# Performance work log

Hardware: AMD Instinct MI355X
Metric: run time of the kernel (lower is better)

Reference implementation:

```python
import jax, jax.numpy as jnp
import numpy as np

B, L, D, T, V, H = 32, 48, 768, 32, 30522, 768

def build_iou_mask_map():
    # Faithful to the __init__ construction: banded validity mask [32, 33].
    m = np.zeros((32, 33), dtype=np.float32)
    for i in range(0, 32, 1):
        m[i, i + 1:min(i + 17, 33)] = 1.0
    for i in range(0, 32 - 16, 2):
        m[i, list(range(18 + i, 33, 2))] = 1.0
    return jnp.asarray(m)

def setup_inputs() -> dict:
    key = jax.random.key(0)
    ks = jax.random.split(key, 6)
    s = 0.02  # xavier-ish init scale
    return {
        'hidden_states_text': jax.random.normal(ks[0], (B, L, D), jnp.float32),
        'hidden_states_object': jax.random.normal(ks[1], (B, T + 1, D), jnp.float32),
        'w_t1': jax.random.normal(ks[2], (D, H), jnp.float32) * s,
        'b_t1': jnp.zeros((H,), jnp.float32),
        'w_t2': jax.random.normal(ks[3], (H, V), jnp.float32) * s,
        'b_t2': jnp.zeros((V,), jnp.float32),
        'w_i1': jax.random.normal(ks[4], (3 * D, H), jnp.float32) * s,
        'b_i1': jnp.zeros((H,), jnp.float32),
        'w_i2': jax.random.normal(ks[5], (H, 3), jnp.float32) * s,
        'b_i2': jnp.zeros((3,), jnp.float32),
    }

def reference(hidden_states_text, hidden_states_object,
              w_t1, b_t1, w_t2, b_t2, w_i1, b_i1, w_i2, b_i2):
    # final_mlp: Dropout(eval: id) -> Linear -> ReLU -> Dropout -> Linear
    logits_text = jax.nn.relu(hidden_states_text @ w_t1 + b_t1) @ w_t2 + b_t2  # [B,L,V]

    hc = hidden_states_object                # [B, T+1, D]
    t = hc.shape[1] - 1
    s_idx = jnp.arange(t)                    # [T]
    e_idx = jnp.arange(t + 1)                # [T+1]
    # (0.5*(s+e)).long() == floor division for non-negative ints
    c_idx = (s_idx[:, None] + e_idx[None, :]) // 2          # [T, T+1]
    c_point = hc[:, c_idx, :]                                # [B, T, T+1, D] gather
    d = hc.shape[-1]
    s_pts = jnp.broadcast_to(hc[:, :-1, None, :], (hc.shape[0], t, t + 1, d))
    e_pts = jnp.broadcast_to(hc[:, None, :, :], (hc.shape[0], t, t + 1, d))
    sce = jnp.concatenate([s_pts, c_point, e_pts], axis=-1)  # [B, T, T+1, 3D]

    # final_mlp_3: Linear(3D->H) -> ReLU -> Dropout(id) -> Linear(H->3)
    h = jax.nn.relu(jnp.einsum('bstf,fh->bsth', sce, w_i1) + b_i1)
    logits_iou = jnp.einsum('bsth,hk->bstk', h, w_i2) + b_i2  # [B,T,T+1,3]
    logits_iou = jnp.transpose(logits_iou, (0, 3, 1, 2))      # [B,3,T,T+1]

    return logits_text, logits_iou, build_iou_mask_map()
```

## Files before the change

### kernel.cpp

```cpp
#include <hip/hip_runtime.h>

typedef unsigned short u16;
typedef short v8s __attribute__((ext_vector_type(8)));
typedef float v4f __attribute__((ext_vector_type(4)));

#define KDIM 768
#define M_TEXT 1536
#define N_VOCAB 30522
#define N_VOCAB_PAD 30592
#define M_HC 1056
#define M_HC_PAD 1152
#define N_IOU 2304
#define OUT_IOU_OFF 46881792
#define OUT_MASK_OFF 46983168

__device__ __forceinline__ u16 f2bf(float f) {
  unsigned u = __float_as_uint(f);
  u += 0x7fffu + ((u >> 16) & 1u);
  return (u16)(u >> 16);
}

__global__ __launch_bounds__(256) void prep_cvt(const float* __restrict__ xt_in,
                                                const float* __restrict__ hc_in,
                                                u16* __restrict__ xt,
                                                u16* __restrict__ hcb,
                                                float* __restrict__ out) {
  const int NXT = M_TEXT * KDIM / 4;
  if (blockIdx.x >= 2016) {
    int idx = (blockIdx.x - 2016) * 256 + threadIdx.x;
    if (idx >= 1056) return;
    int i = idx / 33, j = idx % 33;
    float v = 0.f;
    int hi = min(i + 17, 33);
    if (j >= i + 1 && j < hi) v = 1.f;
    if ((i & 1) == 0 && i < 16 && j >= 18 + i && ((j - (18 + i)) & 1) == 0) v = 1.f;
    out[OUT_MASK_OFF + idx] = v;
    return;
  }
  int i = blockIdx.x * 256 + threadIdx.x;
  if (i < NXT) {
    float4 v = ((const float4*)xt_in)[i];
    ushort4 o; o.x = f2bf(v.x); o.y = f2bf(v.y); o.z = f2bf(v.z); o.w = f2bf(v.w);
    ((ushort4*)xt)[i] = o;
  } else {
    int j = i - NXT;
    int row = j / 192;
    float4 v = make_float4(0.f, 0.f, 0.f, 0.f);
    if (row < M_HC) v = ((const float4*)hc_in)[j];
    ushort4 o; o.x = f2bf(v.x); o.y = f2bf(v.y); o.z = f2bf(v.z); o.w = f2bf(v.w);
    ((ushort4*)hcb)[j] = o;
  }
}

__global__ __launch_bounds__(256) void transpose_all(const float* __restrict__ w_t1,
                                                     u16* __restrict__ w_t1T,
                                                     const float* __restrict__ w_t2,
                                                     u16* __restrict__ w_t2T,
                                                     const float* __restrict__ w_i1,
                                                     u16* __restrict__ w_i1T) {
  __shared__ float tile[64][65];
  int b = blockIdx.x;
  const float* ip; u16* op; int C, bx, by;
  if (b < 144) {
    ip = w_t1; op = w_t1T; C = 768; bx = b % 12; by = b / 12;
  } else if (b < 5880) {
    int r = b - 144; ip = w_t2; op = w_t2T; C = N_VOCAB; bx = r % 12; by = r / 12;
  } else {
    int r = b - 5880; int z = r / 144; int q = r % 144;
    ip = w_i1 + (long)z * 768 * 768; op = w_i1T + (long)z * 768 * 768;
    C = 768; bx = q % 12; by = q / 12;
  }
  int r0 = bx * 64, c0 = by * 64;
  int tx = threadIdx.x & 63, tg = threadIdx.x >> 6;
#pragma unroll
  for (int i = 0; i < 16; ++i) {
    int r = tg + i * 4;
    int gc = c0 + tx;
    tile[r][tx] = (gc < C) ? ip[(long)(r0 + r) * C + gc] : 0.f;
  }
  __syncthreads();
#pragma unroll
  for (int i = 0; i < 16; ++i) {
    int cc = tg + i * 4;
    op[(long)(c0 + cc) * KDIM + r0 + tx] = f2bf(tile[tx][cc]);
  }
}

__global__ __launch_bounds__(256)
void gemm_small(const u16* __restrict__ xt, const u16* __restrict__ w_t1T,
                u16* __restrict__ htext, const float* __restrict__ b_t1,
                const u16* __restrict__ hcb, const u16* __restrict__ w_i1T,
                float* __restrict__ Xcat) {
  __shared__ u16 sA[128 * 32];
  __shared__ u16 sB[128 * 32];
  const int b = blockIdx.x;
  const u16 *A, *BT;
  float* fout = nullptr;
  u16* bfout = nullptr;
  const float* bias = nullptr;
  int mode, bx, by, ldc;
  if (b < 72) {
    mode = 1; bx = b % 6; by = b / 6;
    A = xt; BT = w_t1T; bfout = htext; bias = b_t1; ldc = KDIM;
  } else {
    int r = b - 72;
    mode = 2; bx = r % 18; by = r / 18;
    A = hcb; BT = w_i1T; fout = Xcat; ldc = N_IOU;
  }
  const int tid = threadIdx.x;
  const int wid = tid >> 6;
  const int lane = tid & 63;
  const int lrow = lane & 15;
  const int quad = lane >> 4;
  const int wm = (wid & 1) * 64;
  const int wn = (wid >> 1) * 64;
  const int m0 = by * 128;
  const int n0 = bx * 128;

  const int srow = wid * 32 + (lane >> 2);
  const int scol = (lane & 3) * 8;
  const u16* gA = A + (long)(m0 + srow) * KDIM + scol;
  const u16* gB = BT + (long)(n0 + srow) * KDIM + scol;
  u16* lA = &sA[(wid * 32) * 32];
  u16* lB = &sB[(wid * 32) * 32];

  v4f acc[4][4];
#pragma unroll
  for (int i = 0; i < 4; ++i)
#pragma unroll
    for (int j = 0; j < 4; ++j) acc[i][j] = (v4f){0.f, 0.f, 0.f, 0.f};

  const v8s* pA = (const v8s*)sA;
  const v8s* pB = (const v8s*)sB;
  const int ia0 = (wm + lrow) * 4 + quad;
  const int ib0 = (wn + lrow) * 4 + quad;

  for (int kt = 0; kt < KDIM / 32; ++kt) {
    const u16* ga = gA + kt * 32;
    const u16* gb = gB + kt * 32;
    __builtin_amdgcn_global_load_lds((const __attribute__((address_space(1))) void*)ga,
                                     (__attribute__((address_space(3))) void*)lA, 16, 0, 0);
    __builtin_amdgcn_global_load_lds((const __attribute__((address_space(1))) void*)(ga + 16 * KDIM),
                                     (__attribute__((address_space(3))) void*)(lA + 16 * 32), 16, 0, 0);
    __builtin_amdgcn_global_load_lds((const __attribute__((address_space(1))) void*)gb,
                                     (__attribute__((address_space(3))) void*)lB, 16, 0, 0);
    __builtin_amdgcn_global_load_lds((const __attribute__((address_space(1))) void*)(gb + 16 * KDIM),
                                     (__attribute__((address_space(3))) void*)(lB + 16 * 32), 16, 0, 0);
    __syncthreads();

    v8s af[4], bfr[4];
#pragma unroll
    for (int mt = 0; mt < 4; ++mt) af[mt] = pA[ia0 + mt * 64];
#pragma unroll
    for (int nt = 0; nt < 4; ++nt) bfr[nt] = pB[ib0 + nt * 64];
#pragma unroll
    for (int mt = 0; mt < 4; ++mt)
#pragma unroll
      for (int nt = 0; nt < 4; ++nt)
        acc[mt][nt] = __builtin_amdgcn_mfma_f32_16x16x32_bf16(af[mt], bfr[nt], acc[mt][nt], 0, 0, 0);
    __syncthreads();
  }

#pragma unroll
  for (int nt = 0; nt < 4; ++nt) {
    int c = n0 + wn + nt * 16 + lrow;
    float bv = 0.f;
    if (mode == 1) bv = bias[c];
#pragma unroll
    for (int mt = 0; mt < 4; ++mt) {
#pragma unroll
      for (int r = 0; r < 4; ++r) {
        int row = m0 + wm + mt * 16 + quad * 4 + r;
        float v = acc[mt][nt][r] + bv;
        if (mode == 1) {
          bfout[(long)row * ldc + c] = f2bf(fmaxf(v, 0.f));
        } else {
          fout[(long)row * ldc + c] = v;
        }
      }
    }
  }
}

#define DSREAD_B(sB) do {                                                  \
    const u16* _b = (sB) + bBase;                                          \
    _Pragma("unroll")                                                      \
    for (int _nf = 0; _nf < 4; ++_nf) {                                    \
      bfr[_nf][0] = *(const v8s*)(_b + _nf * 1024 + c0);                   \
      bfr[_nf][1] = *(const v8s*)(_b + _nf * 1024 + c1);                   \
    } } while (0)

#define DSREAD_A(sA, q) do {                                               \
    const u16* _a = (sA) + aBase + (q) * 2048;                             \
    af[0][0] = *(const v8s*)(_a + c0);                                     \
    af[0][1] = *(const v8s*)(_a + c1);                                     \
    af[1][0] = *(const v8s*)(_a + 1024 + c0);                              \
    af[1][1] = *(const v8s*)(_a + 1024 + c1);                              \
  } while (0)

#define MFMA_Q(q) do {                                                     \
    _Pragma("unroll")                                                      \
    for (int _m = 0; _m < 2; ++_m)                                         \
      _Pragma("unroll")                                                    \
      for (int _nf = 0; _nf < 4; ++_nf) {                                  \
        acc[2*(q)+_m][_nf] = __builtin_amdgcn_mfma_f32_16x16x32_bf16(      \
            af[_m][0], bfr[_nf][0], acc[2*(q)+_m][_nf], 0, 0, 0);          \
        acc[2*(q)+_m][_nf] = __builtin_amdgcn_mfma_f32_16x16x32_bf16(      \
            af[_m][1], bfr[_nf][1], acc[2*(q)+_m][_nf], 0, 0, 0);          \
      } } while (0)

#define BAR_SB() do { __builtin_amdgcn_s_barrier();                        \
                      __builtin_amdgcn_sched_barrier(0); } while (0)
#define LGKM0() do { asm volatile("s_waitcnt lgkmcnt(0)" ::: "memory");    \
                     __builtin_amdgcn_sched_barrier(0); } while (0)

__global__ __launch_bounds__(512, 2)
void gemm_big(const u16* __restrict__ A, const u16* __restrict__ BT,
              float* __restrict__ out, const float* __restrict__ bias) {
  __shared__ u16 sbuf[2][2][256 * 64];

  const int id = blockIdx.x;
  const int swz = (id & 7) * 90 + (id >> 3);
  const int mt = swz % 6;
  const int nt = swz / 6;
  const int m0 = mt * 256, n0 = nt * 256;

  const int tid = threadIdx.x;
  const int wid = tid >> 6;
  const int lane = tid & 63;
  const int l3 = lane >> 3;
  const int l7 = lane & 7;
  const int lrow = lane & 15;
  const int quad = lane >> 4;
  const int wr = wid >> 2;
  const int wc = wid & 3;

  const int xc = (l7 ^ l3) * 8;
  const u16* Ag = A  + (long)(m0 + wid * 16 + l3) * KDIM + xc;
  const u16* Bg = BT + (long)(n0 + wid * 16 + l3) * KDIM + xc;

  u16* const sA0 = &sbuf[0][0][0];
  u16* const sB0 = &sbuf[0][1][0];
  u16* const sA1 = &sbuf[1][0][0];
  u16* const sB1 = &sbuf[1][1][0];

  auto stageA = [&](u16* sdst, int kt, int h) {
#pragma unroll
    for (int j = 0; j < 2; ++j)
      __builtin_amdgcn_global_load_lds(
          (const __attribute__((address_space(1))) void*)(Ag + (long)kt * 64 +
                                                          (long)((h * 128 + j * 8) * KDIM)),
          (__attribute__((address_space(3))) void*)(sdst + (h * 128 + wid * 16 + j * 8) * 64),
          16, 0, 0);
  };
  auto stageB = [&](u16* sdst, int kt, int h) {
    const int hh = (n0 + h * 128 >= N_VOCAB_PAD) ? 0 : h;
#pragma unroll
    for (int j = 0; j < 2; ++j)
      __builtin_amdgcn_global_load_lds(
          (const __attribute__((address_space(1))) void*)(Bg + (long)kt * 64 +
                                                          (long)((hh * 128 + j * 8) * KDIM)),
          (__attribute__((address_space(3))) void*)(sdst + (h * 128 + wid * 16 + j * 8) * 64),
          16, 0, 0);
  };

  const int aBase = (wr * 128 + lrow) * 64;
  const int bBase = (wc * 64 + lrow) * 64;
  const int xls = (lrow & 7) * 8;
  const int c0 = (quad * 8) ^ xls;
  const int c1 = c0 ^ 32;

  v4f acc[8][4];
#pragma unroll
  for (int i = 0; i < 8; ++i)
#pragma unroll
    for (int j = 0; j < 4; ++j) acc[i][j] = (v4f){0.f, 0.f, 0.f, 0.f};

  v8s bfr[4][2];
  v8s af[2][2];

  stageA(sA0, 0, 0); stageA(sA0, 0, 1);
  stageB(sB0, 0, 0); stageB(sB0, 0, 1);
  stageB(sB1, 1, 0); stageB(sB1, 1, 1);
  asm volatile("s_waitcnt vmcnt(4)" ::: "memory");
  __builtin_amdgcn_sched_barrier(0);
  BAR_SB();

#pragma unroll 1
  for (int it = 0; it < 6; ++it) {
    const int kA1 = 2 * it + 1;
    const int kB0 = 2 * it + 2;
    const int kB1 = 2 * it + 3;
    const bool more = (it < 5);

    DSREAD_B(sB0);
    DSREAD_A(sA0, 0);
    stageA(sA1, kA1, 0);
    __builtin_amdgcn_s_barrier();
    LGKM0();
    __builtin_amdgcn_s_setprio(1); MFMA_Q(0); __builtin_amdgcn_s_setprio(0);
    BAR_SB();

    DSREAD_A(sA0, 1);
    stageA(sA1, kA1, 1);
    __builtin_amdgcn_s_barrier();
    LGKM0();
    __builtin_amdgcn_s_setprio(1); MFMA_Q(1); __builtin_amdgcn_s_setprio(0);
    BAR_SB();

    DSREAD_A(sA0, 2);
    if (more) stageB(sB0, kB0, 0);
    __builtin_amdgcn_s_barrier();
    LGKM0();
    __builtin_amdgcn_s_setprio(1); MFMA_Q(2); __builtin_amdgcn_s_setprio(0);
    BAR_SB();

    DSREAD_A(sA0, 3);
    if (more) stageB(sB0, kB0, 1);
    __builtin_amdgcn_s_barrier();
    LGKM0();
    __builtin_amdgcn_s_setprio(1); MFMA_Q(3); __builtin_amdgcn_s_setprio(0);
    if (more) { asm volatile("s_waitcnt vmcnt(4)" ::: "memory"); }
    else      { asm volatile("s_waitcnt vmcnt(0)" ::: "memory"); }
    __builtin_amdgcn_sched_barrier(0);
    BAR_SB();

    DSREAD_B(sB1);
    DSREAD_A(sA1, 0);
    if (more) stageA(sA0, kB0, 0);
    __builtin_amdgcn_s_barrier();
    LGKM0();
    __builtin_amdgcn_s_setprio(1); MFMA_Q(0); __builtin_amdgcn_s_setprio(0);
    BAR_SB();

    DSREAD_A(sA1, 1);
    if (more) stageA(sA0, kB0, 1);
    __builtin_amdgcn_s_barrier();
    LGKM0();
    __builtin_amdgcn_s_setprio(1); MFMA_Q(1); __builtin_amdgcn_s_setprio(0);
    BAR_SB();

    DSREAD_A(sA1, 2);
    if (more) stageB(sB1, kB1, 0);
    __builtin_amdgcn_s_barrier();
    LGKM0();
    __builtin_amdgcn_s_setprio(1); MFMA_Q(2); __builtin_amdgcn_s_setprio(0);
    BAR_SB();

    DSREAD_A(sA1, 3);
    if (more) stageB(sB1, kB1, 1);
    __builtin_amdgcn_s_barrier();
    LGKM0();
    __builtin_amdgcn_s_setprio(1); MFMA_Q(3); __builtin_amdgcn_s_setprio(0);
    if (more) { asm volatile("s_waitcnt vmcnt(4)" ::: "memory");
                __builtin_amdgcn_sched_barrier(0); }
    BAR_SB();
  }

#pragma unroll
  for (int nf = 0; nf < 4; ++nf) {
    const int c = n0 + wc * 64 + nf * 16 + lrow;
    if (c < N_VOCAB) {
      const float bv = bias[c];
#pragma unroll
      for (int mf = 0; mf < 8; ++mf) {
        const long r0 = m0 + wr * 128 + mf * 16 + quad * 4;
#pragma unroll
        for (int rr = 0; rr < 4; ++rr)
          out[(r0 + rr) * (long)N_VOCAB + c] = acc[mf][nf][rr] + bv;
      }
    }
  }
}

#undef DSREAD_B
#undef DSREAD_A
#undef MFMA_Q
#undef BAR_SB
#undef LGKM0

__global__ __launch_bounds__(256) void iou_combine(const float* __restrict__ Xcat,
                                                   const float* __restrict__ b1,
                                                   const float* __restrict__ w2,
                                                   const float* __restrict__ b2,
                                                   float* __restrict__ out) {
  int gw = (blockIdx.x * 256 + threadIdx.x) >> 6;
  int lane = threadIdx.x & 63;
  if (gw >= 32 * 32 * 33) return;
  int b = gw / 1056;
  int rem = gw % 1056;
  int s = rem / 33;
  int t = rem % 33;
  int cidx = (s + t) >> 1;
  const float* ps = Xcat + (long)(b * 33 + s) * N_IOU;
  const float* pc = Xcat + (long)(b * 33 + cidx) * N_IOU + 768;
  const float* pe = Xcat + (long)(b * 33 + t) * N_IOU + 1536;
  float a0 = 0.f, a1 = 0.f, a2 = 0.f;
#pragma unroll
  for (int j = 0; j < 3; ++j) {
    int h0 = j * 256 + lane * 4;
    float4 vs = *(const float4*)(ps + h0);
    float4 vc = *(const float4*)(pc + h0);
    float4 ve = *(const float4*)(pe + h0);
    float4 vb = *(const float4*)(b1 + h0);
    const float* fs = (const float*)&vs;
    const float* fc = (const float*)&vc;
    const float* fe = (const float*)&ve;
    const float* fb = (const float*)&vb;
#pragma unroll
    for (int c = 0; c < 4; ++c) {
      float v = fmaxf(fs[c] + fc[c] + fe[c] + fb[c], 0.f);
      int h = h0 + c;
      a0 += v * w2[h * 3 + 0];
      a1 += v * w2[h * 3 + 1];
      a2 += v * w2[h * 3 + 2];
    }
  }
#pragma unroll
  for (int off = 32; off > 0; off >>= 1) {
    a0 += __shfl_down(a0, off, 64);
    a1 += __shfl_down(a1, off, 64);
    a2 += __shfl_down(a2, off, 64);
  }
  if (lane == 0) {
    int base = OUT_IOU_OFF + b * 3168 + s * 33 + t;
    out[base + 0 * 1056] = a0 + b2[0];
    out[base + 1 * 1056] = a1 + b2[1];
    out[base + 2 * 1056] = a2 + b2[2];
  }
}

extern "C" void kernel_launch(void* const* d_in, const int* in_sizes, int n_in,
                              void* d_out, int out_size, void* d_ws, size_t ws_size,
                              hipStream_t stream) {
  const float* hst  = (const float*)d_in[0];
  const float* hso  = (const float*)d_in[1];
  const float* w_t1 = (const float*)d_in[2];
  const float* b_t1 = (const float*)d_in[3];
  const float* w_t2 = (const float*)d_in[4];
  const float* b_t2 = (const float*)d_in[5];
  const float* w_i1 = (const float*)d_in[6];
  const float* b_i1 = (const float*)d_in[7];
  const float* w_i2 = (const float*)d_in[8];
  const float* b_i2 = (const float*)d_in[9];
  float* out = (float*)d_out;

  char* ws = (char*)d_ws;
  u16*   w_t2T = (u16*)(ws + 0);
  u16*   xt    = (u16*)(ws + 46989312);
  u16*   w_t1T = (u16*)(ws + 49348608);
  u16*   htext = (u16*)(ws + 50528256);
  u16*   hcb   = (u16*)(ws + 52887552);
  u16*   w_i1T = (u16*)(ws + 54657024);
  float* Xcat  = (float*)(ws + 58195968);

  prep_cvt<<<dim3(2021), dim3(256), 0, stream>>>(hst, hso, xt, hcb, out);
  transpose_all<<<dim3(6312), dim3(256), 0, stream>>>(w_t1, w_t1T, w_t2, w_t2T, w_i1, w_i1T);

  gemm_small<<<dim3(234), dim3(256), 0, stream>>>(xt, w_t1T, htext, b_t1, hcb, w_i1T, Xcat);

  gemm_big<<<dim3(720), dim3(512), 0, stream>>>(htext, w_t2T, out, b_t2);
  iou_combine<<<dim3(8448), dim3(256), 0, stream>>>(Xcat, b_i1, w_i2, b_i2, out);
}
```

Baseline: 506.9 us.

## Merge five launches into three with independent work co-scheduled per kernel

The stages are regrouped by dependency into three launches instead of five. The small weight transposes join the input conversion kernel. The large vocab-weight transpose is placed in the same grid as the small GEMMs. The IoU combine runs as extra blocks of the big text GEMM. This cuts launch gaps and lets independent work fill idle CUs during tail phases, at the cost of mixing block types that compete for resources and of larger shared-memory and register footprints in the merged kernels.

```diff
diff --git a/kernel.cpp b/kernel.cpp
--- a/kernel.cpp
+++ b/kernel.cpp
@@ -20,14 +20,56 @@
   return (u16)(u >> 16);
 }
 
-__global__ __launch_bounds__(256) void prep_cvt(const float* __restrict__ xt_in,
-                                                const float* __restrict__ hc_in,
-                                                u16* __restrict__ xt,
-                                                u16* __restrict__ hcb,
-                                                float* __restrict__ out) {
+__device__ __forceinline__ void transpose_body(const float* __restrict__ ip,
+                                               u16* __restrict__ op,
+                                               int C, int bx, int by,
+                                               float (*tile)[65]) {
+  int r0 = bx * 64, c0 = by * 64;
+  int tx = threadIdx.x & 63, tg = threadIdx.x >> 6;
+#pragma unroll
+  for (int i = 0; i < 16; ++i) {
+    int r = tg + i * 4;
+    int gc = c0 + tx;
+    tile[r][tx] = (gc < C) ? ip[(long)(r0 + r) * C + gc] : 0.f;
+  }
+  __syncthreads();
+#pragma unroll
+  for (int i = 0; i < 16; ++i) {
+    int cc = tg + i * 4;
+    op[(long)(c0 + cc) * KDIM + r0 + tx] = f2bf(tile[tx][cc]);
+  }
+}
+
+__global__ __launch_bounds__(256) void prep_and_smallT(const float* __restrict__ xt_in,
+                                                       const float* __restrict__ hc_in,
+                                                       u16* __restrict__ xt,
+                                                       u16* __restrict__ hcb,
+                                                       float* __restrict__ out,
+                                                       const float* __restrict__ w_t1,
+                                                       u16* __restrict__ w_t1T,
+                                                       const float* __restrict__ w_i1,
+                                                       u16* __restrict__ w_i1T) {
+  __shared__ float tile[64][65];
   const int NXT = M_TEXT * KDIM / 4;
-  if (blockIdx.x >= 2016) {
-    int idx = (blockIdx.x - 2016) * 256 + threadIdx.x;
+  const int b = blockIdx.x;
+  if (b < 2016) {
+    int i = b * 256 + threadIdx.x;
+    if (i < NXT) {
+      float4 v = ((const float4*)xt_in)[i];
+      ushort4 o; o.x = f2bf(v.x); o.y = f2bf(v.y); o.z = f2bf(v.z); o.w = f2bf(v.w);
+      ((ushort4*)xt)[i] = o;
+    } else {
+      int j = i - NXT;
+      int row = j / 192;
+      float4 v = make_float4(0.f, 0.f, 0.f, 0.f);
+      if (row < M_HC) v = ((const float4*)hc_in)[j];
+      ushort4 o; o.x = f2bf(v.x); o.y = f2bf(v.y); o.z = f2bf(v.z); o.w = f2bf(v.w);
+      ((ushort4*)hcb)[j] = o;
+    }
+    return;
+  }
+  if (b < 2021) {
+    int idx = (b - 2016) * 256 + threadIdx.x;
     if (idx >= 1056) return;
     int i = idx / 33, j = idx % 33;
     float v = 0.f;
@@ -37,73 +79,44 @@
     out[OUT_MASK_OFF + idx] = v;
     return;
   }
-  int i = blockIdx.x * 256 + threadIdx.x;
-  if (i < NXT) {
-    float4 v = ((const float4*)xt_in)[i];
-    ushort4 o; o.x = f2bf(v.x); o.y = f2bf(v.y); o.z = f2bf(v.z); o.w = f2bf(v.w);
-    ((ushort4*)xt)[i] = o;
-  } else {
-    int j = i - NXT;
-    int row = j / 192;
-    float4 v = make_float4(0.f, 0.f, 0.f, 0.f);
-    if (row < M_HC) v = ((const float4*)hc_in)[j];
-    ushort4 o; o.x = f2bf(v.x); o.y = f2bf(v.y); o.z = f2bf(v.z); o.w = f2bf(v.w);
-    ((ushort4*)hcb)[j] = o;
-  }
-}
-
-__global__ __launch_bounds__(256) void transpose_all(const float* __restrict__ w_t1,
-                                                     u16* __restrict__ w_t1T,
-                                                     const float* __restrict__ w_t2,
-                                                     u16* __restrict__ w_t2T,
-                                                     const float* __restrict__ w_i1,
-                                                     u16* __restrict__ w_i1T) {
-  __shared__ float tile[64][65];
-  int b = blockIdx.x;
-  const float* ip; u16* op; int C, bx, by;
-  if (b < 144) {
-    ip = w_t1; op = w_t1T; C = 768; bx = b % 12; by = b / 12;
-  } else if (b < 5880) {
-    int r = b - 144; ip = w_t2; op = w_t2T; C = N_VOCAB; bx = r % 12; by = r / 12;
-  } else {
-    int r = b - 5880; int z = r / 144; int q = r % 144;
-    ip = w_i1 + (long)z * 768 * 768; op = w_i1T + (long)z * 768 * 768;
-    C = 768; bx = q % 12; by = q / 12;
-  }
-  int r0 = bx * 64, c0 = by * 64;
-  int tx = threadIdx.x & 63, tg = threadIdx.x >> 6;
-#pragma unroll
-  for (int i = 0; i < 16; ++i) {
-    int r = tg + i * 4;
-    int gc = c0 + tx;
-    tile[r][tx] = (gc < C) ? ip[(long)(r0 + r) * C + gc] : 0.f;
-  }
-  __syncthreads();
-#pragma unroll
-  for (int i = 0; i < 16; ++i) {
-    int cc = tg + i * 4;
-    op[(long)(c0 + cc) * KDIM + r0 + tx] = f2bf(tile[tx][cc]);
+  if (b < 2165) {
+    int r = b - 2021;
+    transpose_body(w_t1, w_t1T, 768, r % 12, r / 12, tile);
+    return;
+  }
+  {
+    int r = b - 2165;
+    int z = r / 144, q = r % 144;
+    transpose_body(w_i1 + (long)z * 768 * 768, w_i1T + (long)z * 768 * 768,
+                   768, q % 12, q / 12, tile);
   }
 }
 
 __global__ __launch_bounds__(256)
-void gemm_small(const u16* __restrict__ xt, const u16* __restrict__ w_t1T,
-                u16* __restrict__ htext, const float* __restrict__ b_t1,
-                const u16* __restrict__ hcb, const u16* __restrict__ w_i1T,
-                float* __restrict__ Xcat) {
-  __shared__ u16 sA[128 * 32];
-  __shared__ u16 sB[128 * 32];
-  const int b = blockIdx.x;
+void midwork(const u16* __restrict__ xt, const u16* __restrict__ w_t1T,
+             u16* __restrict__ htext, const float* __restrict__ b_t1,
+             const u16* __restrict__ hcb, const u16* __restrict__ w_i1T,
+             float* __restrict__ Xcat,
+             const float* __restrict__ w_t2, u16* __restrict__ w_t2T) {
+  __shared__ char smem[64 * 65 * 4];
+  const int blk = blockIdx.x;
+  if (blk >= 234) {
+    int r = blk - 234;
+    transpose_body(w_t2, w_t2T, N_VOCAB, r % 12, r / 12, (float (*)[65])smem);
+    return;
+  }
+  u16* sA = (u16*)smem;
+  u16* sB = (u16*)(smem + 8192);
   const u16 *A, *BT;
   float* fout = nullptr;
   u16* bfout = nullptr;
   const float* bias = nullptr;
   int mode, bx, by, ldc;
-  if (b < 72) {
-    mode = 1; bx = b % 6; by = b / 6;
+  if (blk < 72) {
+    mode = 1; bx = blk % 6; by = blk / 6;
     A = xt; BT = w_t1T; bfout = htext; bias = b_t1; ldc = KDIM;
   } else {
-    int r = b - 72;
+    int r = blk - 72;
     mode = 2; bx = r % 18; by = r / 18;
     A = hcb; BT = w_i1T; fout = Xcat; ldc = N_IOU;
   }
@@ -215,9 +228,62 @@
                      __builtin_amdgcn_sched_barrier(0); } while (0)
 
 __global__ __launch_bounds__(512, 2)
-void gemm_big(const u16* __restrict__ A, const u16* __restrict__ BT,
-              float* __restrict__ out, const float* __restrict__ bias) {
+void bigwork(const u16* __restrict__ A, const u16* __restrict__ BT,
+             float* __restrict__ out, const float* __restrict__ bias,
+             const float* __restrict__ Xcat, const float* __restrict__ b1,
+             const float* __restrict__ w2, const float* __restrict__ b2) {
   __shared__ u16 sbuf[2][2][256 * 64];
+
+  const int tid = threadIdx.x;
+  const int wid = tid >> 6;
+  const int lane = tid & 63;
+
+  if (blockIdx.x >= 720) {
+    int gw = (blockIdx.x - 720) * 8 + wid;
+    if (gw >= 32 * 32 * 33) return;
+    int b = gw / 1056;
+    int rem = gw % 1056;
+    int s = rem / 33;
+    int t = rem % 33;
+    int cidx = (s + t) >> 1;
+    const float* ps = Xcat + (long)(b * 33 + s) * N_IOU;
+    const float* pc = Xcat + (long)(b * 33 + cidx) * N_IOU + 768;
+    const float* pe = Xcat + (long)(b * 33 + t) * N_IOU + 1536;
+    float a0 = 0.f, a1 = 0.f, a2 = 0.f;
+#pragma unroll
+    for (int j = 0; j < 3; ++j) {
+      int h0 = j * 256 + lane * 4;
+      float4 vs = *(const float4*)(ps + h0);
+      float4 vc = *(const float4*)(pc + h0);
+      float4 ve = *(const float4*)(pe + h0);
+      float4 vb = *(const float4*)(b1 + h0);
+      const float* fs = (const float*)&vs;
+      const float* fc = (const float*)&vc;
+      const float* fe = (const float*)&ve;
+      const float* fb = (const float*)&vb;
+#pragma unroll
+      for (int c = 0; c < 4; ++c) {
+        float v = fmaxf(fs[c] + fc[c] + fe[c] + fb[c], 0.f);
+        int h = h0 + c;
+        a0 += v * w2[h * 3 + 0];
+        a1 += v * w2[h * 3 + 1];
+        a2 += v * w2[h * 3 + 2];
+      }
+    }
+#pragma unroll
+    for (int off = 32; off > 0; off >>= 1) {
+      a0 += __shfl_down(a0, off, 64);
+      a1 += __shfl_down(a1, off, 64);
+      a2 += __shfl_down(a2, off, 64);
+    }
+    if (lane == 0) {
+      int base = OUT_IOU_OFF + b * 3168 + s * 33 + t;
+      out[base + 0 * 1056] = a0 + b2[0];
+      out[base + 1 * 1056] = a1 + b2[1];
+      out[base + 2 * 1056] = a2 + b2[2];
+    }
+    return;
+  }
 
   const int id = blockIdx.x;
   const int swz = (id & 7) * 90 + (id >> 3);
@@ -225,9 +291,6 @@
   const int nt = swz / 6;
   const int m0 = mt * 256, n0 = nt * 256;
 
-  const int tid = threadIdx.x;
-  const int wid = tid >> 6;
-  const int lane = tid & 63;
   const int l3 = lane >> 3;
   const int l7 = lane & 7;
   const int lrow = lane & 15;
@@ -378,57 +441,6 @@
 #undef MFMA_Q
 #undef BAR_SB
 #undef LGKM0
-
-__global__ __launch_bounds__(256) void iou_combine(const float* __restrict__ Xcat,
-                                                   const float* __restrict__ b1,
-                                                   const float* __restrict__ w2,
-                                                   const float* __restrict__ b2,
-                                                   float* __restrict__ out) {
-  int gw = (blockIdx.x * 256 + threadIdx.x) >> 6;
-  int lane = threadIdx.x & 63;
-  if (gw >= 32 * 32 * 33) return;
-  int b = gw / 1056;
-  int rem = gw % 1056;
-  int s = rem / 33;
-  int t = rem % 33;
-  int cidx = (s + t) >> 1;
-  const float* ps = Xcat + (long)(b * 33 + s) * N_IOU;
-  const float* pc = Xcat + (long)(b * 33 + cidx) * N_IOU + 768;
-  const float* pe = Xcat + (long)(b * 33 + t) * N_IOU + 1536;
-  float a0 = 0.f, a1 = 0.f, a2 = 0.f;
-#pragma unroll
-  for (int j = 0; j < 3; ++j) {
-    int h0 = j * 256 + lane * 4;
-    float4 vs = *(const float4*)(ps + h0);
-    float4 vc = *(const float4*)(pc + h0);
-    float4 ve = *(const float4*)(pe + h0);
-    float4 vb = *(const float4*)(b1 + h0);
-    const float* fs = (const float*)&vs;
-    const float* fc = (const float*)&vc;
-    const float* fe = (const float*)&ve;
-    const float* fb = (const float*)&vb;
-#pragma unroll
-    for (int c = 0; c < 4; ++c) {
-      float v = fmaxf(fs[c] + fc[c] + fe[c] + fb[c], 0.f);
-      int h = h0 + c;
-      a0 += v * w2[h * 3 + 0];
-      a1 += v * w2[h * 3 + 1];
-      a2 += v * w2[h * 3 + 2];
-    }
-  }
-#pragma unroll
-  for (int off = 32; off > 0; off >>= 1) {
-    a0 += __shfl_down(a0, off, 64);
-    a1 += __shfl_down(a1, off, 64);
-    a2 += __shfl_down(a2, off, 64);
-  }
-  if (lane == 0) {
-    int base = OUT_IOU_OFF + b * 3168 + s * 33 + t;
-    out[base + 0 * 1056] = a0 + b2[0];
-    out[base + 1 * 1056] = a1 + b2[1];
-    out[base + 2 * 1056] = a2 + b2[2];
-  }
-}
 
 extern "C" void kernel_launch(void* const* d_in, const int* in_sizes, int n_in,
                               void* d_out, int out_size, void* d_ws, size_t ws_size,
@@ -454,11 +466,12 @@
   u16*   w_i1T = (u16*)(ws + 54657024);
   float* Xcat  = (float*)(ws + 58195968);
 
-  prep_cvt<<<dim3(2021), dim3(256), 0, stream>>>(hst, hso, xt, hcb, out);
-  transpose_all<<<dim3(6312), dim3(256), 0, stream>>>(w_t1, w_t1T, w_t2, w_t2T, w_i1, w_i1T);
-
-  gemm_small<<<dim3(234), dim3(256), 0, stream>>>(xt, w_t1T, htext, b_t1, hcb, w_i1T, Xcat);
-
-  gemm_big<<<dim3(720), dim3(512), 0, stream>>>(htext, w_t2T, out, b_t2);
-  iou_combine<<<dim3(8448), dim3(256), 0, stream>>>(Xcat, b_i1, w_i2, b_i2, out);
-}
+  prep_and_smallT<<<dim3(2597), dim3(256), 0, stream>>>(
+      hst, hso, xt, hcb, out, w_t1, w_t1T, w_i1, w_i1T);
+
+  midwork<<<dim3(5970), dim3(256), 0, stream>>>(
+      xt, w_t1T, htext, b_t1, hcb, w_i1T, Xcat, w_t2, w_t2T);
+
+  bigwork<<<dim3(4944), dim3(512), 0, stream>>>(
+      htext, w_t2T, out, b_t2, Xcat, b_i1, w_i2, b_i2);
+}
```

Measured after the change: 546.8 us. 1.08x slower.
